# Kernel optimization log

Hardware: AMD Instinct MI355X
Metric: run time of the kernel (lower is better)

The kernel has to match this reference:

```python
import jax, jax.numpy as jnp
import numpy as np

QUERY_DIM = 512
CONTEXT_DIM = 768
HEADS = 8
DIM_HEAD = 64
INNER = HEADS * DIM_HEAD  # 512


def setup_inputs() -> dict:
    key = jax.random.key(0)
    ks = jax.random.split(key, 7)
    b, n, ctx = 8, 4096, 512
    s = 0.02
    return {
        "x": jax.random.normal(ks[0], (b, n, QUERY_DIM), jnp.float32),
        "context": jax.random.normal(ks[1], (b, ctx, CONTEXT_DIM), jnp.float32),
        "w_q": jax.random.normal(ks[2], (QUERY_DIM, INNER), jnp.float32) * s,
        "w_k": jax.random.normal(ks[3], (CONTEXT_DIM, INNER), jnp.float32) * s,
        "w_v": jax.random.normal(ks[4], (CONTEXT_DIM, INNER), jnp.float32) * s,
        "w_out": jax.random.normal(ks[5], (INNER, QUERY_DIM), jnp.float32) * s,
        "b_out": jax.random.normal(ks[6], (QUERY_DIM,), jnp.float32) * s,
    }


def reference(x, context, w_q, w_k, w_v, w_out, b_out):
    b, n, _ = x.shape
    ctx = context.shape[1]
    scale = DIM_HEAD ** -0.5
    # project and split heads: [b, h, len, d]
    q = (x @ w_q).reshape(b, n, HEADS, DIM_HEAD).transpose(0, 2, 1, 3)
    k = (context @ w_k).reshape(b, ctx, HEADS, DIM_HEAD).transpose(0, 2, 1, 3)
    v = (context @ w_v).reshape(b, ctx, HEADS, DIM_HEAD).transpose(0, 2, 1, 3)
    attn = jax.nn.softmax(jnp.einsum("bhnd,bhmd->bhnm", q, k) * scale, axis=-1)
    out = jnp.einsum("bhnm,bhmd->bhnd", attn, v)
    out = out.transpose(0, 2, 1, 3).reshape(b, n, INNER)
    return out @ w_out + b_out
```

## Files before the change

### kernel.cpp

```cpp
#include <hip/hip_runtime.h>
#include <hip/hip_bf16.h>
#include <stdint.h>

typedef __attribute__((ext_vector_type(4)))  float  f32x4;
typedef __attribute__((ext_vector_type(16))) float  f32x16;
typedef __attribute__((ext_vector_type(8)))  short  bf8;
typedef __attribute__((ext_vector_type(4)))  short  bf4;
typedef __attribute__((ext_vector_type(4)))  float  fvec4;
typedef __attribute__((ext_vector_type(4)))  unsigned uvec4;
typedef __attribute__((ext_vector_type(2)))  unsigned uvec2;

#define AS1 __attribute__((address_space(1)))
#define AS3 __attribute__((address_space(3)))

#if __has_builtin(__builtin_amdgcn_exp2f)
#define EXP2(x) __builtin_amdgcn_exp2f(x)
#else
#define EXP2(x) exp2f(x)
#endif

__device__ __forceinline__ short sbf(float f) {
  __hip_bfloat16 h = __float2bfloat16(f);
  return *reinterpret_cast<short*>(&h);
}

__device__ __forceinline__ unsigned pk2(float lo, float hi) {
  unsigned r;
  asm("v_cvt_pk_bf16_f32 %0, %1, %2" : "=v"(r) : "v"(lo), "v"(hi));
  return r;
}

__device__ __forceinline__ void tr_tile(const float* __restrict__ src,
                                        short* __restrict__ dst, int K,
                                        float scale, int kx, int ny) {
  __shared__ short t[64][65];
  const int k0 = kx * 64, n0 = ny * 64;
  const int tx = threadIdx.x & 15, ty = threadIdx.x >> 4;
  #pragma unroll
  for (int i = 0; i < 4; ++i) {
    int k = ty + i * 16;
    fvec4 v = *(const fvec4*)(src + (size_t)(k0 + k) * 512 + n0 + tx * 4);
    t[tx * 4 + 0][k] = sbf(v[0] * scale);
    t[tx * 4 + 1][k] = sbf(v[1] * scale);
    t[tx * 4 + 2][k] = sbf(v[2] * scale);
    t[tx * 4 + 3][k] = sbf(v[3] * scale);
  }
  __syncthreads();
  #pragma unroll
  for (int i = 0; i < 4; ++i) {
    int n = ty + i * 16;
    bf4 o = *(bf4*)&t[n][tx * 4];
    *(bf4*)(dst + (size_t)(n0 + n) * K + k0 + tx * 4) = o;
  }
}

__global__ __launch_bounds__(256)
void prep_weights(const float* __restrict__ wq, const float* __restrict__ wk,
                  const float* __restrict__ wv, const float* __restrict__ wo,
                  short* __restrict__ wqT, short* __restrict__ wkvT,
                  short* __restrict__ woT, float qscale) {
  int bx = blockIdx.x;
  if (bx < 64)        tr_tile(wq, wqT, 512, qscale, bx & 7, bx >> 3);
  else if (bx < 160)  { int l = bx - 64;  tr_tile(wk, wkvT,            768, 1.0f, l % 12, l / 12); }
  else if (bx < 256)  { int l = bx - 160; tr_tile(wv, wkvT + 512*768,  768, 1.0f, l % 12, l / 12); }
  else                { int l = bx - 256; tr_tile(wo, woT, 512, 1.0f, l & 7, l >> 3); }
}

template<int EPI, bool AF32>
__global__ __launch_bounds__(256, 3)
void gemm128(const void* __restrict__ Av, const short* __restrict__ Bt,
             void* __restrict__ Cout, void* __restrict__ Cout2,
             const float* __restrict__ bias, int M, int N, int K) {
  __shared__ short As[2][4096];
  __shared__ short Bs[2][4096];
  const short* A16 = (const short*)Av;
  const float* A32 = (const float*)Av;
  const int tid = threadIdx.x;
  const int w = tid >> 6, l = tid & 63, g = l >> 4, c15 = l & 15;
  const int mbase = blockIdx.x * 128, nbase = blockIdx.y * 128;
  const int wr = (w >> 1) << 6, wc = (w & 1) << 6;

  f32x4 acc[4][4];
  #pragma unroll
  for (int mi = 0; mi < 4; ++mi)
    #pragma unroll
    for (int ni = 0; ni < 4; ++ni) acc[mi][ni] = (f32x4){0.f, 0.f, 0.f, 0.f};

  int rowS[2], loS[2];
  #pragma unroll
  for (int p = 0; p < 2; ++p) {
    int pb = p * 4096 + tid * 16;
    rowS[p] = pb >> 6;
    loS[p] = ((pb & 63) ^ ((rowS[p] & 3) << 4)) >> 1;
  }

  const int ar = tid >> 1, ac0 = (tid & 1) * 16, acl = (tid & 1) * 2;
  short* wdst0 = &As[0][ar * 32 + 8 * ((acl + 0) ^ (ar & 3))];
  short* wdst1 = &As[0][ar * 32 + 8 * ((acl + 1) ^ (ar & 3))];

  auto stageB = [&](int ks, int b) {
    #pragma unroll
    for (int p = 0; p < 2; ++p) {
      const short* gb = Bt + (size_t)(nbase + rowS[p]) * K + (ks << 5) + loS[p];
      __builtin_amdgcn_global_load_lds((const AS1 void*)gb,
          (AS3 void*)(&Bs[b][p * 2048 + w * 512]), 16, 0, 0);
    }
  };
  auto stageA16 = [&](int ks, int b) {
    #pragma unroll
    for (int p = 0; p < 2; ++p) {
      const short* ga = A16 + (size_t)(mbase + rowS[p]) * K + (ks << 5) + loS[p];
      __builtin_amdgcn_global_load_lds((const AS1 void*)ga,
          (AS3 void*)(&As[b][p * 2048 + w * 512]), 16, 0, 0);
    }
  };

  const int nk = K >> 5;
  fvec4 a0, a1, a2, a3;
  auto loadA32 = [&](int ks) {
    const float* p = A32 + (size_t)(mbase + ar) * K + (ks << 5) + ac0;
    a0 = *(const fvec4*)(p);
    a1 = *(const fvec4*)(p + 4);
    a2 = *(const fvec4*)(p + 8);
    a3 = *(const fvec4*)(p + 12);
  };
  auto writeA32 = [&](int b) {
    uvec4 w0, w1;
    w0[0] = pk2(a0[0], a0[1]); w0[1] = pk2(a0[2], a0[3]);
    w0[2] = pk2(a1[0], a1[1]); w0[3] = pk2(a1[2], a1[3]);
    w1[0] = pk2(a2[0], a2[1]); w1[1] = pk2(a2[2], a2[3]);
    w1[2] = pk2(a3[0], a3[1]); w1[3] = pk2(a3[2], a3[3]);
    *(uvec4*)(wdst0 + b * 4096) = w0;
    *(uvec4*)(wdst1 + b * 4096) = w1;
  };

  if (AF32) { loadA32(0); writeA32(0); }
  else      { stageA16(0, 0); }
  stageB(0, 0);

  int buf = 0;
  for (int ks = 0; ks < nk; ++ks) {
    asm volatile("s_waitcnt vmcnt(0) lgkmcnt(0)\ns_barrier" ::: "memory");
    if (ks + 1 < nk) {
      if (AF32) loadA32(ks + 1);
      else      stageA16(ks + 1, buf ^ 1);
      stageB(ks + 1, buf ^ 1);
    }

    bf8 af[4], bfr[4];
    #pragma unroll
    for (int mi = 0; mi < 4; ++mi) {
      int row = wr + mi * 16 + c15;
      af[mi] = *(const bf8*)&As[buf][(row << 5) + ((g << 3) ^ ((row & 3) << 3))];
    }
    #pragma unroll
    for (int ni = 0; ni < 4; ++ni) {
      int row = wc + ni * 16 + c15;
      bfr[ni] = *(const bf8*)&Bs[buf][(row << 5) + ((g << 3) ^ ((row & 3) << 3))];
    }
    #pragma unroll
    for (int mi = 0; mi < 4; ++mi)
      #pragma unroll
      for (int ni = 0; ni < 4; ++ni)
        acc[mi][ni] = __builtin_amdgcn_mfma_f32_16x16x32_bf16(af[mi], bfr[ni], acc[mi][ni], 0, 0, 0);

    if (AF32 && ks + 1 < nk) writeA32(buf ^ 1);
    buf ^= 1;
  }

  if (EPI == 2) {
    short* Kb = (short*)Cout;
    short* Vt = (short*)Cout2;
    #pragma unroll
    for (int mi = 0; mi < 4; ++mi) {
      int row0 = mbase + wr + mi * 16 + (g << 2);
      int b = row0 >> 9, key0 = row0 & 511;
      #pragma unroll
      for (int ni = 0; ni < 4; ++ni) {
        int col = nbase + wc + ni * 16 + c15;
        if (col < 512) {
          int h = col >> 6, d = col & 63;
          size_t base = ((size_t)((b << 3) + h) << 15) + d;
          #pragma unroll
          for (int r = 0; r < 4; ++r)
            Kb[base + ((size_t)(key0 + r) << 6)] = sbf(acc[mi][ni][r]);
        } else {
          int cc = col - 512;
          int h = cc >> 6, d = cc & 63;
          size_t base = ((size_t)((b << 3) + h) << 15) + ((size_t)d << 9) + key0;
          bf4 o4;
          #pragma unroll
          for (int r = 0; r < 4; ++r) o4[r] = sbf(acc[mi][ni][r]);
          *(bf4*)&Vt[base] = o4;
        }
      }
    }
  } else {
    #pragma unroll
    for (int mi = 0; mi < 4; ++mi) {
      int row0 = mbase + wr + mi * 16 + (g << 2);
      #pragma unroll
      for (int ni = 0; ni < 4; ++ni) {
        int col = nbase + wc + ni * 16 + c15;
        #pragma unroll
        for (int r = 0; r < 4; ++r) {
          float v = acc[mi][ni][r];
          if (EPI == 1) {
            v += bias[col];
            ((float*)Cout)[(size_t)(row0 + r) * N + col] = v;
          } else {
            ((short*)Cout)[(size_t)(row0 + r) * N + col] = sbf(v);
          }
        }
      }
    }
  }
}

template<int EPI, bool AF32>
__global__ __launch_bounds__(512, 2)
void gemm256(const void* __restrict__ Av, const short* __restrict__ Bt,
             void* __restrict__ Cout, void* __restrict__ Cout2,
             const float* __restrict__ bias, int M, int N, int K) {
  extern __shared__ short smem[];
  short* As = smem;
  short* Bs = smem + 16384;
  const short* A16 = (const short*)Av;
  const float* A32 = (const float*)Av;
  const int tid = threadIdx.x;
  const int w = tid >> 6, l = tid & 63, g = l >> 4, c15 = l & 15;
  const int mbase = blockIdx.x * 256, nbase = blockIdx.y * 256;
  const int wrM = (w >> 2) * 128, wc = (w & 3) * 64;

  f32x4 acc[8][4];
  #pragma unroll
  for (int mi = 0; mi < 8; ++mi)
    #pragma unroll
    for (int ni = 0; ni < 4; ++ni) acc[mi][ni] = (f32x4){0.f, 0.f, 0.f, 0.f};

  int rowS[2], loS[2];
  #pragma unroll
  for (int p = 0; p < 2; ++p) {
    int pb = p * 8192 + tid * 16;
    rowS[p] = pb >> 6;
    loS[p] = ((pb & 63) ^ ((rowS[p] & 3) << 4)) >> 1;
  }

  const int ar = tid >> 1, ac0 = (tid & 1) * 16, acl = (tid & 1) * 2;
  short* wdst0 = &As[ar * 32 + 8 * ((acl + 0) ^ (ar & 3))];
  short* wdst1 = &As[ar * 32 + 8 * ((acl + 1) ^ (ar & 3))];

  auto stageB = [&](int ks, int b) {
    #pragma unroll
    for (int p = 0; p < 2; ++p) {
      const short* gb = Bt + (size_t)(nbase + rowS[p]) * K + (ks << 5) + loS[p];
      __builtin_amdgcn_global_load_lds((const AS1 void*)gb,
          (AS3 void*)(Bs + b * 8192 + p * 4096 + tid * 8), 16, 0, 0);
    }
  };
  auto stageA16 = [&](int ks, int b) {
    #pragma unroll
    for (int p = 0; p < 2; ++p) {
      const short* ga = A16 + (size_t)(mbase + rowS[p]) * K + (ks << 5) + loS[p];
      __builtin_amdgcn_global_load_lds((const AS1 void*)ga,
          (AS3 void*)(As + b * 8192 + p * 4096 + tid * 8), 16, 0, 0);
    }
  };

  const int nk = K >> 5;
  fvec4 a0, a1, a2, a3;
  auto loadA32 = [&](int ks) {
    const float* p = A32 + (size_t)(mbase + ar) * K + (ks << 5) + ac0;
    a0 = *(const fvec4*)(p);
    a1 = *(const fvec4*)(p + 4);
    a2 = *(const fvec4*)(p + 8);
    a3 = *(const fvec4*)(p + 12);
  };
  auto writeA32 = [&](int b) {
    uvec4 w0, w1;
    w0[0] = pk2(a0[0], a0[1]); w0[1] = pk2(a0[2], a0[3]);
    w0[2] = pk2(a1[0], a1[1]); w0[3] = pk2(a1[2], a1[3]);
    w1[0] = pk2(a2[0], a2[1]); w1[1] = pk2(a2[2], a2[3]);
    w1[2] = pk2(a3[0], a3[1]); w1[3] = pk2(a3[2], a3[3]);
    *(uvec4*)(wdst0 + b * 8192) = w0;
    *(uvec4*)(wdst1 + b * 8192) = w1;
  };

  if (AF32) { loadA32(0); writeA32(0); }
  else      { stageA16(0, 0); }
  stageB(0, 0);

  int buf = 0;
  for (int ks = 0; ks < nk; ++ks) {
    asm volatile("s_waitcnt vmcnt(0) lgkmcnt(0)\ns_barrier" ::: "memory");
    if (ks + 1 < nk) {
      if (AF32) loadA32(ks + 1);
      else      stageA16(ks + 1, buf ^ 1);
      stageB(ks + 1, buf ^ 1);
    }

    bf8 bfr[4];
    #pragma unroll
    for (int ni = 0; ni < 4; ++ni) {
      int row = wc + ni * 16 + c15;
      bfr[ni] = *(const bf8*)&Bs[buf * 8192 + (row << 5) + ((g << 3) ^ ((row & 3) << 3))];
    }
    #pragma unroll
    for (int mi = 0; mi < 8; ++mi) {
      int row = wrM + mi * 16 + c15;
      bf8 af = *(const bf8*)&As[buf * 8192 + (row << 5) + ((g << 3) ^ ((row & 3) << 3))];
      #pragma unroll
      for (int ni = 0; ni < 4; ++ni)
        acc[mi][ni] = __builtin_amdgcn_mfma_f32_16x16x32_bf16(af, bfr[ni], acc[mi][ni], 0, 0, 0);
    }

    if (AF32 && ks + 1 < nk) writeA32(buf ^ 1);
    buf ^= 1;
  }

  #pragma unroll
  for (int mi = 0; mi < 8; ++mi) {
    int row0 = mbase + wrM + mi * 16 + (g << 2);
    #pragma unroll
    for (int ni = 0; ni < 4; ++ni) {
      int col = nbase + wc + ni * 16 + c15;
      #pragma unroll
      for (int r = 0; r < 4; ++r) {
        float v = acc[mi][ni][r];
        if (EPI == 1) {
          v += bias[col];
          ((float*)Cout)[(size_t)(row0 + r) * N + col] = v;
        } else {
          ((short*)Cout)[(size_t)(row0 + r) * N + col] = sbf(v);
        }
      }
    }
  }
}

__global__ __launch_bounds__(512, 4)
void attn_fwd(const short* __restrict__ Q, const short* __restrict__ Kb,
              const short* __restrict__ Vt, short* __restrict__ O) {
  extern __shared__ short smem[];

  const int p = blockIdx.x;
  const int v = (p & 7) * 128 + (p >> 3);
  const int bh = v >> 4, qx = v & 15;
  const int tid = threadIdx.x;
  const int w = tid >> 6, l = tid & 63, q = l & 31, h2 = l >> 5;
  const int bb = bh >> 3, h = bh & 7;
  const size_t orow0 = (size_t)bb * 4096 + qx * 256;
  const size_t kvbase = (size_t)bh << 15;

  bf8 qf[4];
  #pragma unroll
  for (int ds = 0; ds < 4; ++ds)
    qf[ds] = *(const bf8*)(Q + (orow0 + w * 32 + q) * 512 + h * 64 + ds * 16 + 8 * h2);

  const int srow = tid >> 3;
  const int soff = (tid & 7) * 16;
  const int slo  = (soff ^ ((srow & 7) << 4)) >> 1;
  const short* srcK0 = Kb + kvbase + ((size_t)srow << 6) + slo;
  const short* srcV0 = Vt + kvbase + ((size_t)srow << 9) + slo;

#define STAGE(t) do { \
    __builtin_amdgcn_global_load_lds((const AS1 void*)(srcK0 + ((size_t)(t) << 12)), \
        (AS3 void*)(smem + ((t) & 1) * 4096 + tid * 8), 16, 0, 0); \
    __builtin_amdgcn_global_load_lds((const AS1 void*)(srcV0 + ((t) << 6)), \
        (AS3 void*)(smem + 8192 + ((t) & 1) * 4096 + tid * 8), 16, 0, 0); } while (0)

  f32x16 o[2];
  #pragma unroll
  for (int db = 0; db < 2; ++db)
    #pragma unroll
    for (int r = 0; r < 16; ++r) o[db][r] = 0.f;
  float ls0 = 0.f, ls1 = 0.f, ls2 = 0.f, ls3 = 0.f;

  STAGE(0);

  #pragma unroll 2
  for (int t = 0; t < 8; ++t) {
    asm volatile("s_waitcnt vmcnt(0)\ns_barrier" ::: "memory");
    if (t < 7) STAGE(t + 1);
    const short* Kt  = smem + (t & 1) * 4096;
    const short* Vtl = smem + 8192 + (t & 1) * 4096;

    f32x16 s[2];
    __builtin_amdgcn_s_setprio(1);
    #pragma unroll
    for (int kb = 0; kb < 2; ++kb) {
      #pragma unroll
      for (int r = 0; r < 16; ++r) s[kb][r] = 0.f;
      #pragma unroll
      for (int ds = 0; ds < 4; ++ds) {
        bf8 kf = *(const bf8*)&Kt[((kb * 32 + q) << 6) +
                                  ((ds * 16 + 8 * h2) ^ ((q & 7) << 3))];
        s[kb] = __builtin_amdgcn_mfma_f32_32x32x16_bf16(kf, qf[ds], s[kb], 0, 0, 0);
      }
    }
    __builtin_amdgcn_s_setprio(0);

    #pragma unroll
    for (int kb = 0; kb < 2; ++kb)
      #pragma unroll
      for (int r = 0; r < 16; r += 4) {
        float p0 = EXP2(s[kb][r]);
        float p1 = EXP2(s[kb][r + 1]);
        float p2 = EXP2(s[kb][r + 2]);
        float p3 = EXP2(s[kb][r + 3]);
        s[kb][r] = p0; s[kb][r + 1] = p1; s[kb][r + 2] = p2; s[kb][r + 3] = p3;
        ls0 += p0; ls1 += p1; ls2 += p2; ls3 += p3;
      }

    #pragma unroll
    for (int ks = 0; ks < 4; ++ks) {
      const int kb = ks >> 1, rb = (ks & 1) * 8;
      unsigned X = pk2(s[kb][rb + 0], s[kb][rb + 1]);
      unsigned Y = pk2(s[kb][rb + 2], s[kb][rb + 3]);
      unsigned Z = pk2(s[kb][rb + 4], s[kb][rb + 5]);
      unsigned W = pk2(s[kb][rb + 6], s[kb][rb + 7]);
      asm volatile("v_permlane32_swap_b32 %0, %1" : "+v"(X), "+v"(Z));
      asm volatile("v_permlane32_swap_b32 %0, %1" : "+v"(Y), "+v"(W));
      union { unsigned u[4]; bf8 b; } pf;
      pf.u[0] = X; pf.u[1] = Y; pf.u[2] = Z; pf.u[3] = W;
      __builtin_amdgcn_s_setprio(1);
      #pragma unroll
      for (int db = 0; db < 2; ++db) {
        bf8 vf = *(const bf8*)&Vtl[((db * 32 + q) << 6) +
                                   ((ks * 16 + 8 * h2) ^ ((q & 7) << 3))];
        o[db] = __builtin_amdgcn_mfma_f32_32x32x16_bf16(vf, pf.b, o[db], 0, 0, 0);
      }
      __builtin_amdgcn_s_setprio(0);
    }
  }
#undef STAGE

  float lsum = (ls0 + ls1) + (ls2 + ls3);
  float tot = lsum + __shfl_xor(lsum, 32);
  float rs = 1.0f / tot;
  short* Orow = O + (orow0 + w * 32 + q) * 512 + h * 64;
  #pragma unroll
  for (int db = 0; db < 2; ++db)
    #pragma unroll
    for (int rq = 0; rq < 4; ++rq) {
      int r = rq * 4;
      uvec2 u;
      u[0] = pk2(o[db][r] * rs,     o[db][r + 1] * rs);
      u[1] = pk2(o[db][r + 2] * rs, o[db][r + 3] * rs);
      *(uvec2*)&Orow[db * 32 + rq * 8 + h2 * 4] = u;
    }
}

extern "C" void kernel_launch(void* const* d_in, const int* in_sizes, int n_in,
                              void* d_out, int out_size, void* d_ws, size_t ws_size,
                              hipStream_t stream) {
  const float* x   = (const float*)d_in[0];
  const float* ctx = (const float*)d_in[1];
  const float* wq  = (const float*)d_in[2];
  const float* wk  = (const float*)d_in[3];
  const float* wv  = (const float*)d_in[4];
  const float* wo  = (const float*)d_in[5];
  const float* bo  = (const float*)d_in[6];
  float* out = (float*)d_out;

  char* ws = (char*)d_ws;
  short* wqT  = (short*)(ws + 39845888);
  short* wkvT = (short*)(ws + 40370176);
  short* woT  = (short*)(ws + 41943040);
  short* Qb   = (short*)(ws + 42467328);
  short* Kbf  = (short*)(ws + 76021760);
  short* Vtf  = (short*)(ws + 80216064);
  short* Ab   = (short*)(ws + 84410368);

  (void)hipFuncSetAttribute((const void*)attn_fwd,
                            hipFuncAttributeMaxDynamicSharedMemorySize, 32768);
  (void)hipFuncSetAttribute((const void*)gemm256<0, true>,
                            hipFuncAttributeMaxDynamicSharedMemorySize, 65536);
  (void)hipFuncSetAttribute((const void*)gemm256<1, false>,
                            hipFuncAttributeMaxDynamicSharedMemorySize, 65536);

  const float QSCALE = 0.18033688011f;

  prep_weights<<<320, 256, 0, stream>>>(wq, wk, wv, wo, wqT, wkvT, woT, QSCALE);

  gemm256<0, true><<<dim3(128, 2), 512, 65536, stream>>>(x, wqT, Qb, nullptr, nullptr, 32768, 512, 512);
  gemm128<2, true><<<dim3(32, 8), 256, 0, stream>>>(ctx, wkvT, Kbf, Vtf, nullptr, 4096, 1024, 768);
  attn_fwd<<<dim3(1024), 512, 32768, stream>>>(Qb, Kbf, Vtf, Ab);
  gemm256<1, false><<<dim3(128, 2), 512, 65536, stream>>>(Ab, woT, out, nullptr, bo, 32768, 512, 512);
}
```

Measured before the change: 137.7 us.

## Fuse Q and KV projection GEMMs into one 128-tile launch

Replaces the separate gemm256 Q projection and gemm128 KV projection launches with a single qkv_fused kernel of 1280 blocks. The first 256 blocks compute K/V with a swizzled block order and the rest compute Q using 128x128 tiles. This removes one launch and lets the smaller KV work overlap with Q work to fill the GPU. In exchange, the Q GEMM moves from 256x256 tiles to 128x128 tiles, which lowers data reuse per block.

```diff
diff --git a/kernel.cpp b/kernel.cpp
--- a/kernel.cpp
+++ b/kernel.cpp
@@ -66,18 +66,30 @@
   else                { int l = bx - 256; tr_tile(wo, woT, 512, 1.0f, l & 7, l >> 3); }
 }
 
-template<int EPI, bool AF32>
 __global__ __launch_bounds__(256, 3)
-void gemm128(const void* __restrict__ Av, const short* __restrict__ Bt,
-             void* __restrict__ Cout, void* __restrict__ Cout2,
-             const float* __restrict__ bias, int M, int N, int K) {
+void qkv_fused(const float* __restrict__ x, const short* __restrict__ wqT,
+               short* __restrict__ Qb,
+               const float* __restrict__ ctx, const short* __restrict__ wkvT,
+               short* __restrict__ Kbf, short* __restrict__ Vtf) {
   __shared__ short As[2][4096];
   __shared__ short Bs[2][4096];
-  const short* A16 = (const short*)Av;
-  const float* A32 = (const float*)Av;
   const int tid = threadIdx.x;
   const int w = tid >> 6, l = tid & 63, g = l >> 4, c15 = l & 15;
-  const int mbase = blockIdx.x * 128, nbase = blockIdx.y * 128;
+
+  const int p = blockIdx.x;
+  const bool isKV = (p < 256);
+  const float* A32;
+  const short* Bt;
+  int K, mbase, nbase;
+  if (isKV) {
+    int vv = (p & 7) * 32 + (p >> 3);
+    mbase = (vv >> 3) * 128; nbase = (vv & 7) * 128;
+    K = 768; A32 = ctx; Bt = wkvT;
+  } else {
+    int ql = p - 256;
+    mbase = (ql >> 2) * 128; nbase = (ql & 3) * 128;
+    K = 512; A32 = x; Bt = wqT;
+  }
   const int wr = (w >> 1) << 6, wc = (w & 1) << 6;
 
   f32x4 acc[4][4];
@@ -88,10 +100,10 @@
 
   int rowS[2], loS[2];
   #pragma unroll
-  for (int p = 0; p < 2; ++p) {
-    int pb = p * 4096 + tid * 16;
-    rowS[p] = pb >> 6;
-    loS[p] = ((pb & 63) ^ ((rowS[p] & 3) << 4)) >> 1;
+  for (int pp = 0; pp < 2; ++pp) {
+    int pb = pp * 4096 + tid * 16;
+    rowS[pp] = pb >> 6;
+    loS[pp] = ((pb & 63) ^ ((rowS[pp] & 3) << 4)) >> 1;
   }
 
   const int ar = tid >> 1, ac0 = (tid & 1) * 16, acl = (tid & 1) * 2;
@@ -100,29 +112,20 @@
 
   auto stageB = [&](int ks, int b) {
     #pragma unroll
-    for (int p = 0; p < 2; ++p) {
-      const short* gb = Bt + (size_t)(nbase + rowS[p]) * K + (ks << 5) + loS[p];
+    for (int pp = 0; pp < 2; ++pp) {
+      const short* gb = Bt + (size_t)(nbase + rowS[pp]) * K + (ks << 5) + loS[pp];
       __builtin_amdgcn_global_load_lds((const AS1 void*)gb,
-          (AS3 void*)(&Bs[b][p * 2048 + w * 512]), 16, 0, 0);
-    }
-  };
-  auto stageA16 = [&](int ks, int b) {
-    #pragma unroll
-    for (int p = 0; p < 2; ++p) {
-      const short* ga = A16 + (size_t)(mbase + rowS[p]) * K + (ks << 5) + loS[p];
-      __builtin_amdgcn_global_load_lds((const AS1 void*)ga,
-          (AS3 void*)(&As[b][p * 2048 + w * 512]), 16, 0, 0);
-    }
-  };
-
-  const int nk = K >> 5;
+          (AS3 void*)(&Bs[b][pp * 2048 + w * 512]), 16, 0, 0);
+    }
+  };
+
   fvec4 a0, a1, a2, a3;
   auto loadA32 = [&](int ks) {
-    const float* p = A32 + (size_t)(mbase + ar) * K + (ks << 5) + ac0;
-    a0 = *(const fvec4*)(p);
-    a1 = *(const fvec4*)(p + 4);
-    a2 = *(const fvec4*)(p + 8);
-    a3 = *(const fvec4*)(p + 12);
+    const float* pa = A32 + (size_t)(mbase + ar) * K + (ks << 5) + ac0;
+    a0 = *(const fvec4*)(pa);
+    a1 = *(const fvec4*)(pa + 4);
+    a2 = *(const fvec4*)(pa + 8);
+    a3 = *(const fvec4*)(pa + 12);
   };
   auto writeA32 = [&](int b) {
     uvec4 w0, w1;
@@ -134,16 +137,15 @@
     *(uvec4*)(wdst1 + b * 4096) = w1;
   };
 
-  if (AF32) { loadA32(0); writeA32(0); }
-  else      { stageA16(0, 0); }
+  const int nk = K >> 5;
+  loadA32(0); writeA32(0);
   stageB(0, 0);
 
   int buf = 0;
   for (int ks = 0; ks < nk; ++ks) {
     asm volatile("s_waitcnt vmcnt(0) lgkmcnt(0)\ns_barrier" ::: "memory");
     if (ks + 1 < nk) {
-      if (AF32) loadA32(ks + 1);
-      else      stageA16(ks + 1, buf ^ 1);
+      loadA32(ks + 1);
       stageB(ks + 1, buf ^ 1);
     }
 
@@ -164,13 +166,11 @@
       for (int ni = 0; ni < 4; ++ni)
         acc[mi][ni] = __builtin_amdgcn_mfma_f32_16x16x32_bf16(af[mi], bfr[ni], acc[mi][ni], 0, 0, 0);
 
-    if (AF32 && ks + 1 < nk) writeA32(buf ^ 1);
+    if (ks + 1 < nk) writeA32(buf ^ 1);
     buf ^= 1;
   }
 
-  if (EPI == 2) {
-    short* Kb = (short*)Cout;
-    short* Vt = (short*)Cout2;
+  if (isKV) {
     #pragma unroll
     for (int mi = 0; mi < 4; ++mi) {
       int row0 = mbase + wr + mi * 16 + (g << 2);
@@ -183,7 +183,7 @@
           size_t base = ((size_t)((b << 3) + h) << 15) + d;
           #pragma unroll
           for (int r = 0; r < 4; ++r)
-            Kb[base + ((size_t)(key0 + r) << 6)] = sbf(acc[mi][ni][r]);
+            Kbf[base + ((size_t)(key0 + r) << 6)] = sbf(acc[mi][ni][r]);
         } else {
           int cc = col - 512;
           int h = cc >> 6, d = cc & 63;
@@ -191,7 +191,7 @@
           bf4 o4;
           #pragma unroll
           for (int r = 0; r < 4; ++r) o4[r] = sbf(acc[mi][ni][r]);
-          *(bf4*)&Vt[base] = o4;
+          *(bf4*)&Vtf[base] = o4;
         }
       }
     }
@@ -203,15 +203,8 @@
       for (int ni = 0; ni < 4; ++ni) {
         int col = nbase + wc + ni * 16 + c15;
         #pragma unroll
-        for (int r = 0; r < 4; ++r) {
-          float v = acc[mi][ni][r];
-          if (EPI == 1) {
-            v += bias[col];
-            ((float*)Cout)[(size_t)(row0 + r) * N + col] = v;
-          } else {
-            ((short*)Cout)[(size_t)(row0 + r) * N + col] = sbf(v);
-          }
-        }
+        for (int r = 0; r < 4; ++r)
+          Qb[(size_t)(row0 + r) * 512 + col] = sbf(acc[mi][ni][r]);
       }
     }
   }
@@ -474,8 +467,6 @@
 
   (void)hipFuncSetAttribute((const void*)attn_fwd,
                             hipFuncAttributeMaxDynamicSharedMemorySize, 32768);
-  (void)hipFuncSetAttribute((const void*)gemm256<0, true>,
-                            hipFuncAttributeMaxDynamicSharedMemorySize, 65536);
   (void)hipFuncSetAttribute((const void*)gemm256<1, false>,
                             hipFuncAttributeMaxDynamicSharedMemorySize, 65536);
 
@@ -483,8 +474,7 @@
 
   prep_weights<<<320, 256, 0, stream>>>(wq, wk, wv, wo, wqT, wkvT, woT, QSCALE);
 
-  gemm256<0, true><<<dim3(128, 2), 512, 65536, stream>>>(x, wqT, Qb, nullptr, nullptr, 32768, 512, 512);
-  gemm128<2, true><<<dim3(32, 8), 256, 0, stream>>>(ctx, wkvT, Kbf, Vtf, nullptr, 4096, 1024, 768);
+  qkv_fused<<<dim3(1280), 256, 0, stream>>>(x, wqT, Qb, ctx, wkvT, Kbf, Vtf);
   attn_fwd<<<dim3(1024), 512, 32768, stream>>>(Qb, Kbf, Vtf, Ab);
   gemm256<1, false><<<dim3(128, 2), 512, 65536, stream>>>(Ab, woT, out, nullptr, bo, 32768, 512, 512);
 }
```

Measured after the change: 141.9 us. 3.0% more time.
